# Performance work log

Hardware: AMD Instinct MI355X
Metric: run time of the kernel (lower is better)

Reference implementation:

```python
import jax, jax.numpy as jnp
import numpy as np


def _slice_coeffs(grid, guide):
    """Trilinear slice of bilateral grid at (x, y, guide) per full-res pixel.
    grid:  [B, C, D, Hg, Wg]  (C=12 affine coeffs)
    guide: [B, 1, H, W] in [0, 1]
    returns coeffs [B, C, H, W]
    """
    B, C, D, Hg, Wg = grid.shape
    H, W = guide.shape[2], guide.shape[3]
    g = guide[:, 0]  # [B, H, W]

    # HDRNet sampling convention: pixel centers mapped into grid coords
    gx = (jnp.arange(W, dtype=grid.dtype) + 0.5) / W * Wg - 0.5   # [W]
    gy = (jnp.arange(H, dtype=grid.dtype) + 0.5) / H * Hg - 0.5   # [H]
    gz = g * D - 0.5                                              # [B, H, W]

    gx = jnp.broadcast_to(gx[None, None, :], (B, H, W))
    gy = jnp.broadcast_to(gy[None, :, None], (B, H, W))

    fx0 = jnp.floor(gx); fy0 = jnp.floor(gy); fz0 = jnp.floor(gz)
    wx = gx - fx0; wy = gy - fy0; wz = gz - fz0  # trilinear fractions

    x0 = jnp.clip(fx0.astype(jnp.int32), 0, Wg - 1)
    x1 = jnp.clip(fx0.astype(jnp.int32) + 1, 0, Wg - 1)
    y0 = jnp.clip(fy0.astype(jnp.int32), 0, Hg - 1)
    y1 = jnp.clip(fy0.astype(jnp.int32) + 1, 0, Hg - 1)
    z0 = jnp.clip(fz0.astype(jnp.int32), 0, D - 1)
    z1 = jnp.clip(fz0.astype(jnp.int32) + 1, 0, D - 1)

    def gather_one(gb, zi, yi, xi):
        # gb: [C, D, Hg, Wg]; zi/yi/xi: [H, W] -> [C, H, W]
        return gb[:, zi, yi, xi]

    gather = jax.vmap(gather_one)  # over batch

    out = jnp.zeros((B, C, H, W), dtype=grid.dtype)
    for zi, wzc in ((z0, 1.0 - wz), (z1, wz)):
        for yi, wyc in ((y0, 1.0 - wy), (y1, wy)):
            for xi, wxc in ((x0, 1.0 - wx), (x1, wx)):
                w = (wzc * wyc * wxc)[:, None]  # [B, 1, H, W]
                out = out + w * gather(grid, zi, yi, xi)
    return out


def setup_inputs() -> dict:
    key = jax.random.key(0)
    k1, k2, k3 = jax.random.split(key, 3)
    Bilterial_Grid = jax.random.normal(k1, (4, 12, 8, 16, 16), dtype=jnp.float32)
    Guide = jax.random.uniform(k2, (4, 1, 1024, 1024), dtype=jnp.float32)
    fr = jax.random.uniform(k3, (4, 3, 1024, 1024), dtype=jnp.float32)
    return {"Bilterial_Grid": Bilterial_Grid, "Guide": Guide, "fr": fr}


def reference(Bilterial_Grid, Guide, fr):
    B, _, H, W = fr.shape
    coeffs = _slice_coeffs(Bilterial_Grid, Guide)          # [B, 12, H, W]
    co = coeffs.reshape(B, 3, 4, H, W)                      # 3x4 affine per pixel
    # out_c = sum_i A[c,i] * fr_i + b[c]
    out = jnp.einsum('boihw,bihw->bohw', co[:, :, :3], fr) + co[:, :, 3]
    return out
```

## Files before the change

### kernel.cpp

```cpp
#include <hip/hip_runtime.h>


#define ZSTRIDE 100

using half2v = decltype(__builtin_amdgcn_cvt_pkrtz(0.0f, 0.0f));

static __device__ __forceinline__ half2v pkrtz(float lo, float hi) {
    return __builtin_amdgcn_cvt_pkrtz(lo, hi);
}
static __device__ __forceinline__ half2v u2h2(unsigned int u) {
    return __builtin_bit_cast(half2v, u);
}
static __device__ __forceinline__ unsigned int h2u(half2v h) {
    return __builtin_bit_cast(unsigned int, h);
}

#if __has_builtin(__builtin_amdgcn_fdot2)
#define DOT2(d, wp, acc) __builtin_amdgcn_fdot2(u2h2(d), (wp), (acc), false)
#else
static __device__ __forceinline__ float dot2_sw(unsigned int d, half2v wp, float acc) {
    half2v h = u2h2(d);
    return fmaf((float)wp.x, (float)h.x, fmaf((float)wp.y, (float)h.y, acc));
}
#define DOT2(d, wp, acc) dot2_sw((d), (wp), (acc))
#endif

static __device__ __forceinline__ void corner_dot(
    const unsigned int* __restrict__ cp, half2v wp,
    float& a0, float& a1, float& a2, float& a3)
{
    const uint4 d = *reinterpret_cast<const uint4*>(cp);
    a0 = DOT2(d.x, wp, a0);
    a1 = DOT2(d.y, wp, a1);
    a2 = DOT2(d.z, wp, a2);
    a3 = DOT2(d.w, wp, a3);
}

static __device__ __forceinline__ void px_eval(
    const unsigned int* __restrict__ lds,
    float g, float f0, float f1, float f2,
    float u0, float u1, float v0, float v1,
    int cof0, int cof1, int cof2, int cof3,
    float& o0, float& o1, float& o2)
{
    const float gz = g * 8.0f - 0.5f;
    int s = (int)floorf(gz);
    s = min(max(s, 0), 7);
    const float wz = fmaxf(gz - (float)s, 0.0f);
    const float zl = 1.0f - wz, zh = wz;
    const unsigned int* sb = &lds[s * ZSTRIDE];

    const float w00 = v0 * u0, w01 = v0 * u1;
    const float w10 = v1 * u0, w11 = v1 * u1;
    const half2v wp0 = pkrtz(w00 * zl, w00 * zh);
    const half2v wp1 = pkrtz(w01 * zl, w01 * zh);
    const half2v wp2 = pkrtz(w10 * zl, w10 * zh);
    const half2v wp3 = pkrtz(w11 * zl, w11 * zh);

    {
        float a0 = 0.f, a1 = 0.f, a2 = 0.f, a3 = 0.f;
        corner_dot(sb + cof0, wp0, a0, a1, a2, a3);
        corner_dot(sb + cof1, wp1, a0, a1, a2, a3);
        corner_dot(sb + cof2, wp2, a0, a1, a2, a3);
        corner_dot(sb + cof3, wp3, a0, a1, a2, a3);
        o0 = fmaf(a0, f0, fmaf(a1, f1, fmaf(a2, f2, a3)));
    }
    {
        float a0 = 0.f, a1 = 0.f, a2 = 0.f, a3 = 0.f;
        corner_dot(sb + cof0 + 4, wp0, a0, a1, a2, a3);
        corner_dot(sb + cof1 + 4, wp1, a0, a1, a2, a3);
        corner_dot(sb + cof2 + 4, wp2, a0, a1, a2, a3);
        corner_dot(sb + cof3 + 4, wp3, a0, a1, a2, a3);
        o1 = fmaf(a0, f0, fmaf(a1, f1, fmaf(a2, f2, a3)));
    }
    {
        float a0 = 0.f, a1 = 0.f, a2 = 0.f, a3 = 0.f;
        corner_dot(sb + cof0 + 8, wp0, a0, a1, a2, a3);
        corner_dot(sb + cof1 + 8, wp1, a0, a1, a2, a3);
        corner_dot(sb + cof2 + 8, wp2, a0, a1, a2, a3);
        corner_dot(sb + cof3 + 8, wp3, a0, a1, a2, a3);
        o2 = fmaf(a0, f0, fmaf(a1, f1, fmaf(a2, f2, a3)));
    }
}

__global__ __launch_bounds__(256, 5) void slice_apply(
    const float* __restrict__ grid,
    const float* __restrict__ guide,
    const float* __restrict__ fr,
    float* __restrict__ out)
{
    __shared__ __align__(16) unsigned int lds[8 * ZSTRIDE];

    const int b     = blockIdx.y;
    const int tileX = blockIdx.x & 15;
    const int tileY = blockIdx.x >> 4;
    const int t     = threadIdx.x;

    const int w   = t >> 6;
    const int l   = t & 63;
    const int by  = w >> 1;
    const int bx  = w & 1;
    const int lx2 = l & 15;
    const int sub = l >> 4;

    const int txA = bx * 32 + lx2 * 2;
    const int xg  = tileX * 64 + txA;
    const int y0  = tileY * 32 + by * 16 + sub;
    int gofs = (b * 1024 + y0) * 1024 + xg;
    int fofs = ((b * 3) * 1024 + y0) * 1024 + xg;

    float2 gv  = *reinterpret_cast<const float2*>(guide + gofs);
    float2 f0v = *reinterpret_cast<const float2*>(fr + fofs);
    float2 f1v = *reinterpret_cast<const float2*>(fr + fofs + 1048576);
    float2 f2v = *reinterpret_cast<const float2*>(fr + fofs + 2097152);

    {
        const int yodd = tileY & 1;
        const int fy0  = (tileY >> 1) - 1 + yodd;
        const int ry0  = min(max(fy0, 0), 15);
        const int ry1  = min(max(fy0 + 1, 0), 15);
        const int px0  = min(max(tileX - 1, 0), 15);
        const int px1  = tileX;
        const int px2  = min(tileX + 1, 15);
        for (int e = t; e < 8 * 6 * 12; e += 256) {
            const int c    = e % 12;
            const int cell = (e / 12) % 6;
            const int s    = e / 72;
            const int s2   = min(s + 1, 7);
            const int yr   = cell / 3;
            const int xc   = cell % 3;
            const int ry = yr ? ry1 : ry0;
            const int rx = (xc == 0) ? px0 : ((xc == 1) ? px1 : px2);
            const int cb = (b * 12 + c) * 8;
            const int sp = ry * 16 + rx;
            const float lo = grid[(cb + s)  * 256 + sp];
            const float hi = grid[(cb + s2) * 256 + sp];
            lds[s * ZSTRIDE + cell * 12 + c] = h2u(pkrtz(lo, hi));
        }
    }
    __syncthreads();

    const float wxA = ((float)txA + 0.5f) * 0.015625f + (0.5f - (float)bx);
    const float wxB = wxA + 0.015625f;
    const float u1A = wxA, u0A = 1.0f - wxA;
    const float u1B = wxB, u0B = 1.0f - wxB;

    const int cof0 = (0 + bx) * 12;
    const int cof1 = (1 + bx) * 12;
    const int cof2 = (3 + bx) * 12;
    const int cof3 = (4 + bx) * 12;

    const float wyb = (tileY & 1) ? 0.0f : 0.5f;

    #pragma unroll
    for (int i = 0; i < 4; ++i) {
        float2 gn = gv, f0n = f0v, f1n = f1v, f2n = f2v;
        if (i < 3) {
            const int gofs_n = gofs + 4 * 1024;
            const int fofs_n = fofs + 4 * 1024;
            gn  = *reinterpret_cast<const float2*>(guide + gofs_n);
            f0n = *reinterpret_cast<const float2*>(fr + fofs_n);
            f1n = *reinterpret_cast<const float2*>(fr + fofs_n + 1048576);
            f2n = *reinterpret_cast<const float2*>(fr + fofs_n + 2097152);
        }

        const int ly = by * 16 + i * 4 + sub;
        const float wy = ((float)ly + 0.5f) * 0.015625f + wyb;
        const float v1 = wy, v0 = 1.0f - wy;

        float oA0, oA1, oA2, oB0, oB1, oB2;
        px_eval(lds, gv.x, f0v.x, f1v.x, f2v.x, u0A, u1A, v0, v1,
                cof0, cof1, cof2, cof3, oA0, oA1, oA2);
        px_eval(lds, gv.y, f0v.y, f1v.y, f2v.y, u0B, u1B, v0, v1,
                cof0, cof1, cof2, cof3, oB0, oB1, oB2);

        *reinterpret_cast<float2*>(out + fofs)           = make_float2(oA0, oB0);
        *reinterpret_cast<float2*>(out + fofs + 1048576) = make_float2(oA1, oB1);
        *reinterpret_cast<float2*>(out + fofs + 2097152) = make_float2(oA2, oB2);

        gofs += 4 * 1024;
        fofs += 4 * 1024;
        gv = gn; f0v = f0n; f1v = f1n; f2v = f2n;
    }
}

extern "C" void kernel_launch(void* const* d_in, const int* in_sizes, int n_in,
                              void* d_out, int out_size, void* d_ws, size_t ws_size,
                              hipStream_t stream) {
    const float* grid  = (const float*)d_in[0];
    const float* guide = (const float*)d_in[1];
    const float* fr    = (const float*)d_in[2];
    float* out = (float*)d_out;

    dim3 g(512, 4);
    dim3 blk(256);
    hipLaunchKernelGGL(slice_apply, g, blk, 0, stream, grid, guide, fr, out);
}
```

Measured before the change: 120.7 us.

## Switch to one pixel per thread with scalar loads and higher occupancy

Each thread now handles one pixel per row iteration instead of two adjacent pixels, using scalar loads and stores in place of float2. The loop runs eight non-unrolled iterations of two rows each, and the manual software prefetch of the next row's inputs is removed. Launch bounds raise the occupancy target from 5 to 8 blocks per CU to hide memory latency through more resident waves instead of explicit prefetching. The cost is narrower memory transactions and less per-thread memory parallelism.

```diff
diff --git a/kernel.cpp b/kernel.cpp
--- a/kernel.cpp
+++ b/kernel.cpp
@@ -36,54 +36,7 @@
     a3 = DOT2(d.w, wp, a3);
 }
 
-static __device__ __forceinline__ void px_eval(
-    const unsigned int* __restrict__ lds,
-    float g, float f0, float f1, float f2,
-    float u0, float u1, float v0, float v1,
-    int cof0, int cof1, int cof2, int cof3,
-    float& o0, float& o1, float& o2)
-{
-    const float gz = g * 8.0f - 0.5f;
-    int s = (int)floorf(gz);
-    s = min(max(s, 0), 7);
-    const float wz = fmaxf(gz - (float)s, 0.0f);
-    const float zl = 1.0f - wz, zh = wz;
-    const unsigned int* sb = &lds[s * ZSTRIDE];
-
-    const float w00 = v0 * u0, w01 = v0 * u1;
-    const float w10 = v1 * u0, w11 = v1 * u1;
-    const half2v wp0 = pkrtz(w00 * zl, w00 * zh);
-    const half2v wp1 = pkrtz(w01 * zl, w01 * zh);
-    const half2v wp2 = pkrtz(w10 * zl, w10 * zh);
-    const half2v wp3 = pkrtz(w11 * zl, w11 * zh);
-
-    {
-        float a0 = 0.f, a1 = 0.f, a2 = 0.f, a3 = 0.f;
-        corner_dot(sb + cof0, wp0, a0, a1, a2, a3);
-        corner_dot(sb + cof1, wp1, a0, a1, a2, a3);
-        corner_dot(sb + cof2, wp2, a0, a1, a2, a3);
-        corner_dot(sb + cof3, wp3, a0, a1, a2, a3);
-        o0 = fmaf(a0, f0, fmaf(a1, f1, fmaf(a2, f2, a3)));
-    }
-    {
-        float a0 = 0.f, a1 = 0.f, a2 = 0.f, a3 = 0.f;
-        corner_dot(sb + cof0 + 4, wp0, a0, a1, a2, a3);
-        corner_dot(sb + cof1 + 4, wp1, a0, a1, a2, a3);
-        corner_dot(sb + cof2 + 4, wp2, a0, a1, a2, a3);
-        corner_dot(sb + cof3 + 4, wp3, a0, a1, a2, a3);
-        o1 = fmaf(a0, f0, fmaf(a1, f1, fmaf(a2, f2, a3)));
-    }
-    {
-        float a0 = 0.f, a1 = 0.f, a2 = 0.f, a3 = 0.f;
-        corner_dot(sb + cof0 + 8, wp0, a0, a1, a2, a3);
-        corner_dot(sb + cof1 + 8, wp1, a0, a1, a2, a3);
-        corner_dot(sb + cof2 + 8, wp2, a0, a1, a2, a3);
-        corner_dot(sb + cof3 + 8, wp3, a0, a1, a2, a3);
-        o2 = fmaf(a0, f0, fmaf(a1, f1, fmaf(a2, f2, a3)));
-    }
-}
-
-__global__ __launch_bounds__(256, 5) void slice_apply(
+__global__ __launch_bounds__(256, 8) void slice_apply(
     const float* __restrict__ grid,
     const float* __restrict__ guide,
     const float* __restrict__ fr,
@@ -95,24 +48,6 @@
     const int tileX = blockIdx.x & 15;
     const int tileY = blockIdx.x >> 4;
     const int t     = threadIdx.x;
-
-    const int w   = t >> 6;
-    const int l   = t & 63;
-    const int by  = w >> 1;
-    const int bx  = w & 1;
-    const int lx2 = l & 15;
-    const int sub = l >> 4;
-
-    const int txA = bx * 32 + lx2 * 2;
-    const int xg  = tileX * 64 + txA;
-    const int y0  = tileY * 32 + by * 16 + sub;
-    int gofs = (b * 1024 + y0) * 1024 + xg;
-    int fofs = ((b * 3) * 1024 + y0) * 1024 + xg;
-
-    float2 gv  = *reinterpret_cast<const float2*>(guide + gofs);
-    float2 f0v = *reinterpret_cast<const float2*>(fr + fofs);
-    float2 f1v = *reinterpret_cast<const float2*>(fr + fofs + 1048576);
-    float2 f2v = *reinterpret_cast<const float2*>(fr + fofs + 2097152);
 
     {
         const int yodd = tileY & 1;
@@ -140,10 +75,21 @@
     }
     __syncthreads();
 
-    const float wxA = ((float)txA + 0.5f) * 0.015625f + (0.5f - (float)bx);
-    const float wxB = wxA + 0.015625f;
-    const float u1A = wxA, u0A = 1.0f - wxA;
-    const float u1B = wxB, u0B = 1.0f - wxB;
+    const int w   = t >> 6;
+    const int l   = t & 63;
+    const int by  = w >> 1;
+    const int bx  = w & 1;
+    const int lx  = l & 31;
+    const int sub = l >> 5;
+
+    const int tx  = bx * 32 + lx;
+    const int xg  = tileX * 64 + tx;
+    const int y0  = tileY * 32 + by * 16 + sub;
+    int gofs = (b * 1024 + y0) * 1024 + xg;
+    int fofs = ((b * 3) * 1024 + y0) * 1024 + xg;
+
+    const float wx = ((float)tx + 0.5f) * 0.015625f + (0.5f - (float)bx);
+    const float u1 = wx, u0 = 1.0f - wx;
 
     const int cof0 = (0 + bx) * 12;
     const int cof1 = (1 + bx) * 12;
@@ -152,35 +98,63 @@
 
     const float wyb = (tileY & 1) ? 0.0f : 0.5f;
 
-    #pragma unroll
-    for (int i = 0; i < 4; ++i) {
-        float2 gn = gv, f0n = f0v, f1n = f1v, f2n = f2v;
-        if (i < 3) {
-            const int gofs_n = gofs + 4 * 1024;
-            const int fofs_n = fofs + 4 * 1024;
-            gn  = *reinterpret_cast<const float2*>(guide + gofs_n);
-            f0n = *reinterpret_cast<const float2*>(fr + fofs_n);
-            f1n = *reinterpret_cast<const float2*>(fr + fofs_n + 1048576);
-            f2n = *reinterpret_cast<const float2*>(fr + fofs_n + 2097152);
-        }
+    #pragma unroll 1
+    for (int i = 0; i < 8; ++i) {
+        const float g  = guide[gofs];
+        const float f0 = fr[fofs];
+        const float f1 = fr[fofs + 1048576];
+        const float f2 = fr[fofs + 2097152];
 
-        const int ly = by * 16 + i * 4 + sub;
+        const int ly = by * 16 + i * 2 + sub;
         const float wy = ((float)ly + 0.5f) * 0.015625f + wyb;
         const float v1 = wy, v0 = 1.0f - wy;
 
-        float oA0, oA1, oA2, oB0, oB1, oB2;
-        px_eval(lds, gv.x, f0v.x, f1v.x, f2v.x, u0A, u1A, v0, v1,
-                cof0, cof1, cof2, cof3, oA0, oA1, oA2);
-        px_eval(lds, gv.y, f0v.y, f1v.y, f2v.y, u0B, u1B, v0, v1,
-                cof0, cof1, cof2, cof3, oB0, oB1, oB2);
+        const float gz = g * 8.0f - 0.5f;
+        int s = (int)floorf(gz);
+        s = min(max(s, 0), 7);
+        const float wz = fmaxf(gz - (float)s, 0.0f);
+        const float zl = 1.0f - wz, zh = wz;
+        const unsigned int* sb = &lds[s * ZSTRIDE];
 
-        *reinterpret_cast<float2*>(out + fofs)           = make_float2(oA0, oB0);
-        *reinterpret_cast<float2*>(out + fofs + 1048576) = make_float2(oA1, oB1);
-        *reinterpret_cast<float2*>(out + fofs + 2097152) = make_float2(oA2, oB2);
+        const float w00 = v0 * u0, w01 = v0 * u1;
+        const float w10 = v1 * u0, w11 = v1 * u1;
+        const half2v wp0 = pkrtz(w00 * zl, w00 * zh);
+        const half2v wp1 = pkrtz(w01 * zl, w01 * zh);
+        const half2v wp2 = pkrtz(w10 * zl, w10 * zh);
+        const half2v wp3 = pkrtz(w11 * zl, w11 * zh);
 
-        gofs += 4 * 1024;
-        fofs += 4 * 1024;
-        gv = gn; f0v = f0n; f1v = f1n; f2v = f2n;
+        float o0, o1, o2;
+        {
+            float a0 = 0.f, a1 = 0.f, a2 = 0.f, a3 = 0.f;
+            corner_dot(sb + cof0, wp0, a0, a1, a2, a3);
+            corner_dot(sb + cof1, wp1, a0, a1, a2, a3);
+            corner_dot(sb + cof2, wp2, a0, a1, a2, a3);
+            corner_dot(sb + cof3, wp3, a0, a1, a2, a3);
+            o0 = fmaf(a0, f0, fmaf(a1, f1, fmaf(a2, f2, a3)));
+        }
+        {
+            float a0 = 0.f, a1 = 0.f, a2 = 0.f, a3 = 0.f;
+            corner_dot(sb + cof0 + 4, wp0, a0, a1, a2, a3);
+            corner_dot(sb + cof1 + 4, wp1, a0, a1, a2, a3);
+            corner_dot(sb + cof2 + 4, wp2, a0, a1, a2, a3);
+            corner_dot(sb + cof3 + 4, wp3, a0, a1, a2, a3);
+            o1 = fmaf(a0, f0, fmaf(a1, f1, fmaf(a2, f2, a3)));
+        }
+        {
+            float a0 = 0.f, a1 = 0.f, a2 = 0.f, a3 = 0.f;
+            corner_dot(sb + cof0 + 8, wp0, a0, a1, a2, a3);
+            corner_dot(sb + cof1 + 8, wp1, a0, a1, a2, a3);
+            corner_dot(sb + cof2 + 8, wp2, a0, a1, a2, a3);
+            corner_dot(sb + cof3 + 8, wp3, a0, a1, a2, a3);
+            o2 = fmaf(a0, f0, fmaf(a1, f1, fmaf(a2, f2, a3)));
+        }
+
+        out[fofs]           = o0;
+        out[fofs + 1048576] = o1;
+        out[fofs + 2097152] = o2;
+
+        gofs += 2 * 1024;
+        fofs += 2 * 1024;
     }
 }
 
```

Result: no change. 119.4 us (-1.1%).
